# Performance work log

Hardware: AMD Instinct MI355X
Metric: run time of the kernel (lower is better)

The kernel has to match this reference:

```python
import jax, jax.numpy as jnp
import numpy as np

D_MODEL = 1024
D_HIDDEN = 4096
N_EXPERTS = 8
B, S = 2, 2048


def setup_inputs() -> dict:
    key = jax.random.key(0)
    ks = jax.random.split(key, 4)
    sd = 1.0 / np.sqrt(D_MODEL)
    sh = 1.0 / np.sqrt(D_HIDDEN)
    return {
        "x": jax.random.normal(ks[0], (B, S, D_MODEL), dtype=jnp.float32),
        "Wg": jax.random.normal(ks[1], (D_MODEL, N_EXPERTS), dtype=jnp.float32) * sd,
        "bg": jnp.zeros((N_EXPERTS,), dtype=jnp.float32),
        "W1": jax.random.normal(ks[2], (N_EXPERTS, D_MODEL, D_HIDDEN), dtype=jnp.float32) * sd,
        "b1": jnp.zeros((N_EXPERTS, D_HIDDEN), dtype=jnp.float32),
        "W2": jax.random.normal(ks[3], (N_EXPERTS, D_HIDDEN, D_MODEL), dtype=jnp.float32) * sh,
        "b2": jnp.zeros((N_EXPERTS, D_MODEL), dtype=jnp.float32),
    }


def reference(x, Wg, bg, W1, b1, W2, b2):
    # Router: softmax is monotone, so argmax(softmax(logits)) == argmax(logits).
    logits = jnp.einsum("bsd,de->bse", x, Wg) + bg
    expert_idx = jnp.argmax(logits, axis=-1)  # [B, S]
    # Top-1 dispatch, expressed as compute-all-experts + per-token select
    # (jit-friendly; the torch loop masks/gathers per expert).
    h = jax.nn.gelu(jnp.einsum("bsd,edh->bseh", x, W1) + b1, approximate=False)
    y = jnp.einsum("bseh,ehd->bsed", h, W2) + b2  # [B, S, E, D]
    out = jnp.take_along_axis(y, expert_idx[:, :, None, None], axis=2)[:, :, 0, :]
    return out
```

## Files before the change

### kernel.cpp

```cpp
#include <hip/hip_runtime.h>
#include <hip/hip_bf16.h>
#include <math.h>

#define D_MODEL 1024
#define D_HIDDEN 4096
#define N_EXP 8
#define N_TOK 4096
#define MBS 40

typedef __attribute__((ext_vector_type(8))) __bf16 bf16x8_t;
typedef __attribute__((ext_vector_type(4))) float f32x4_t;

#define WS_PREFIX_OFF 128
#define WS_BUCKET_OFF 256
#define WS_XB_OFF     ((size_t)1 << 18)
#define WS_HT_OFF     (((size_t)1 << 18) + ((size_t)8 << 20))
#define WS_W1T_OFF    (((size_t)1 << 18) + ((size_t)50 << 20))
#define WS_W2T_OFF    (((size_t)1 << 18) + ((size_t)114 << 20))
#define WS_AE_OFF     (((size_t)1 << 18) + ((size_t)178 << 20))
#define WS_NEED       (((size_t)1 << 18) + ((size_t)189 << 20))

__device__ __forceinline__ void gload16(const void* g, void* l) {
    __builtin_amdgcn_global_load_lds(
        (__attribute__((address_space(1))) void*)(g),
        (__attribute__((address_space(3))) void*)(l),
        16, 0, 0);
}

__global__ __launch_bounds__(64) void init_counts(int* counts) {
    if (threadIdx.x < N_EXP) counts[threadIdx.x] = 0;
}

__global__ __launch_bounds__(64) void prefix_kernel(const int* counts, int* prefix) {
    if (threadIdx.x == 0) {
        int s = 0;
        prefix[0] = 0;
#pragma unroll
        for (int e = 0; e < N_EXP; ++e) { s += (counts[e] + 127) >> 7; prefix[e + 1] = s; }
    }
}

__global__ __launch_bounds__(256) void router_kernel(
    const float* __restrict__ x, const float* __restrict__ Wg,
    const float* __restrict__ bg, int* __restrict__ counts,
    int* __restrict__ bucket, __hip_bfloat16* __restrict__ xb)
{
    const int wid  = threadIdx.x >> 6;
    const int lane = threadIdx.x & 63;
    const int t    = blockIdx.x * 4 + wid;
    const float* xr = x + (size_t)t * D_MODEL;

    double acc[N_EXP];
#pragma unroll
    for (int e = 0; e < N_EXP; ++e) acc[e] = 0.0;

#pragma unroll
    for (int j = 0; j < D_MODEL / 64; ++j) {
        const int d = j * 64 + lane;
        const float xv = xr[d];
        xb[(size_t)t * D_MODEL + d] = __float2bfloat16(xv);
        const float4* wr = (const float4*)(Wg + (size_t)d * N_EXP);
        const float4 w0 = wr[0], w1 = wr[1];
        const double xd = (double)xv;
        acc[0] += xd * (double)w0.x; acc[1] += xd * (double)w0.y;
        acc[2] += xd * (double)w0.z; acc[3] += xd * (double)w0.w;
        acc[4] += xd * (double)w1.x; acc[5] += xd * (double)w1.y;
        acc[6] += xd * (double)w1.z; acc[7] += xd * (double)w1.w;
    }
#pragma unroll
    for (int e = 0; e < N_EXP; ++e) {
        double v = acc[e];
#pragma unroll
        for (int off = 32; off >= 1; off >>= 1) v += __shfl_xor(v, off, 64);
        acc[e] = v + (double)bg[e];
    }
    if (lane == 0) {
        int best = 0; double bv = acc[0];
#pragma unroll
        for (int e = 1; e < N_EXP; ++e)
            if (acc[e] > bv) { bv = acc[e]; best = e; }
        const int pos = atomicAdd(&counts[best], 1);
        bucket[best * N_TOK + pos] = t;
    }
}

template<int KT, int NT>
__global__ __launch_bounds__(256) void convert_w(
    const float* __restrict__ W, __hip_bfloat16* __restrict__ Wt)
{
    constexpr int NB = NT / 128, KC = KT / 64;
    const int nblk = blockIdx.x, kc = blockIdx.y, e = blockIdx.z;
    const int k0 = kc * 64, n0 = nblk * 128;
    const int tid = threadIdx.x;
    __shared__ __hip_bfloat16 Lt[128 * 72];

    const int kr = tid >> 2;
    const int cq = tid & 3;
    const float* src = W + (size_t)e * KT * NT + (size_t)(k0 + kr) * NT + n0 + cq * 32;
#pragma unroll
    for (int f = 0; f < 8; ++f) {
        const float4 v = *(const float4*)(src + f * 4);
#pragma unroll
        for (int j = 0; j < 4; ++j) {
            const int n = cq * 32 + f * 4 + j;
            *(__hip_bfloat16*)((char*)Lt + (size_t)n * 144 + kr * 2) = __float2bfloat16(((const float*)&v)[j]);
        }
    }
    __syncthreads();

    char* outc = (char*)Wt + (((size_t)e * NB + nblk) * KC + kc) * 16384;
    const int n = tid >> 1, half = tid & 1;
#pragma unroll
    for (int s = 0; s < 4; ++s) {
        const int slot = half * 4 + s;
        const int ko = slot ^ (n & 7);
        const uint4 v = *(const uint4*)((const char*)Lt + (size_t)n * 144 + ko * 16);
        *(uint4*)(outc + (size_t)n * 128 + slot * 16) = v;
    }
}

__global__ __launch_bounds__(256) void gather_a(
    const float* __restrict__ x, const int* __restrict__ counts,
    const int* __restrict__ prefix, const int* __restrict__ bucket,
    __hip_bfloat16* __restrict__ Ae)
{
    const int mbg = blockIdx.x, kc = blockIdx.y;
    if (mbg >= prefix[8]) return;
    int e = 0;
#pragma unroll
    for (int q = 1; q < 8; ++q) if (mbg >= prefix[q]) e = q;
    const int cnt  = counts[e];
    const int mblk = mbg - prefix[e];
    const int tid  = threadIdx.x;
    const int m = tid >> 1, half = tid & 1;
    int idx = mblk * 128 + m;
    if (idx >= cnt) idx = cnt - 1;
    const int tok = bucket[e * N_TOK + idx];
    const float* src = x + (size_t)tok * D_MODEL + kc * 64 + half * 32;
    char* dst = (char*)Ae + ((size_t)mbg * 16 + kc) * 16384 + (size_t)m * 128;
#pragma unroll
    for (int s = 0; s < 4; ++s) {
        const float4 a = *(const float4*)(src + s * 8);
        const float4 b = *(const float4*)(src + s * 8 + 4);
        union { __hip_bfloat16 hh[8]; uint4 u; } pk;
#pragma unroll
        for (int j = 0; j < 4; ++j) {
            pk.hh[j]     = __float2bfloat16(((const float*)&a)[j]);
            pk.hh[j + 4] = __float2bfloat16(((const float*)&b)[j]);
        }
        const int ko = half * 4 + s;
        *(uint4*)(dst + ((ko ^ (m & 7)) << 4)) = pk.u;
    }
}

template<int K_TOT, int N_TOT, bool IS_FFN1>
__global__ __launch_bounds__(256, 4) void ffn_gemm_c(
    const __hip_bfloat16* __restrict__ At,
    const __hip_bfloat16* __restrict__ Wt,
    const float* __restrict__ bias,
    const int* __restrict__ counts,
    const int* __restrict__ prefix,
    const int* __restrict__ bucket,
    __hip_bfloat16* __restrict__ hout,
    float* __restrict__ yout)
{
    constexpr int NB  = N_TOT / 128;
    constexpr int KC  = K_TOT / 64;
    constexpr int NWG = MBS * NB;

    const int orig = blockIdx.x;
    const int wg   = (orig & 7) * (NWG >> 3) + (orig >> 3);
    const int nblk = wg / MBS;
    const int mbg  = wg % MBS;
    if (mbg >= prefix[8]) return;
    int e = 0;
#pragma unroll
    for (int q = 1; q < 8; ++q) if (mbg >= prefix[q]) e = q;
    const int cnt = counts[e];
    const int m0  = (mbg - prefix[e]) * 128;
    const int n0  = nblk * 128;

    const int tid  = threadIdx.x;
    const int lane = tid & 63;
    const int wid  = tid >> 6;
    const int wm   = wid >> 1, wn = wid & 1;

    __shared__ char As[16384];
    __shared__ char Bs[16384];
    __shared__ int s_tok[128];

    if (!IS_FFN1 && tid < 128) {
        int idx = m0 + tid;
        if (idx >= cnt) idx = cnt - 1;
        s_tok[tid] = bucket[e * N_TOK + idx];
    }

    const char* Abase = (const char*)At + (size_t)mbg * KC * 16384;
    const char* Bbase = (const char*)Wt + ((size_t)e * NB + nblk) * (size_t)KC * 16384;
    const int off  = wid * 4096 + lane * 16;
    char* lA = As + wid * 4096;
    char* lB = Bs + wid * 4096;

    f32x4_t acc[4][4];
#pragma unroll
    for (int f = 0; f < 4; ++f)
#pragma unroll
        for (int g = 0; g < 4; ++g) acc[f][g] = (f32x4_t){0.f, 0.f, 0.f, 0.f};

    for (int t = 0; t < KC; ++t) {
        const char* Ac = Abase + (size_t)t * 16384 + off;
        const char* Bc = Bbase + (size_t)t * 16384 + off;
#pragma unroll
        for (int i = 0; i < 4; ++i) gload16(Ac + i * 1024, lA + i * 1024);
#pragma unroll
        for (int i = 0; i < 4; ++i) gload16(Bc + i * 1024, lB + i * 1024);
        __syncthreads();

#pragma unroll
        for (int kk = 0; kk < 2; ++kk) {
            uint4 af[4], bf[4];
            const int ko = kk * 4 + (lane >> 4);
#pragma unroll
            for (int f = 0; f < 4; ++f) {
                const int r = wm * 64 + f * 16 + (lane & 15);
                af[f] = *(const uint4*)(As + r * 128 + ((ko ^ (r & 7)) << 4));
            }
#pragma unroll
            for (int g = 0; g < 4; ++g) {
                const int n = wn * 64 + g * 16 + (lane & 15);
                bf[g] = *(const uint4*)(Bs + n * 128 + ((ko ^ (n & 7)) << 4));
            }
#pragma unroll
            for (int f = 0; f < 4; ++f)
#pragma unroll
                for (int g = 0; g < 4; ++g)
                    acc[f][g] = __builtin_amdgcn_mfma_f32_16x16x32_bf16(
                        __builtin_bit_cast(bf16x8_t, af[f]),
                        __builtin_bit_cast(bf16x8_t, bf[g]),
                        acc[f][g], 0, 0, 0);
        }
        __syncthreads();
    }

    if (IS_FFN1) {
        char* hb = (char*)hout + (size_t)mbg * (D_HIDDEN / 64) * 16384;
#pragma unroll
        for (int f = 0; f < 4; ++f) {
#pragma unroll
            for (int j = 0; j < 4; ++j) {
                const int m = wm * 64 + f * 16 + (lane >> 4) * 4 + j;
#pragma unroll
                for (int g = 0; g < 4; ++g) {
                    const int col = n0 + wn * 64 + g * 16 + (lane & 15);
                    float v = acc[f][g][j] + bias[e * N_TOT + col];
                    v = 0.5f * v * (1.0f + erff(v * 0.70710678118654752f));
                    const int kc = col >> 6, kw = col & 63, ko = kw >> 3, b = kw & 7;
                    *(__hip_bfloat16*)(hb + ((size_t)kc * 128 + m) * 128 +
                                       (((ko ^ (m & 7)) << 4) + (b << 1))) = __float2bfloat16(v);
                }
            }
        }
    } else {
#pragma unroll
        for (int f = 0; f < 4; ++f) {
#pragma unroll
            for (int j = 0; j < 4; ++j) {
                const int rl = wm * 64 + f * 16 + (lane >> 4) * 4 + j;
                const bool ok = (m0 + rl) < cnt;
                const int tok = s_tok[rl];
#pragma unroll
                for (int g = 0; g < 4; ++g) {
                    const int col = n0 + wn * 64 + g * 16 + (lane & 15);
                    const float v = acc[f][g][j] + bias[e * N_TOT + col];
                    if (ok) yout[(size_t)tok * N_TOT + col] = v;
                }
            }
        }
    }
}

template<int K_TOT, int N_TOT, bool IS_FFN1>
__global__ __launch_bounds__(256, 2) void ffn_gemm_f32(
    const __hip_bfloat16* __restrict__ A,
    const float* __restrict__ W,
    const float* __restrict__ bias,
    const int* __restrict__ counts,
    const int* __restrict__ bucket,
    __hip_bfloat16* __restrict__ hout,
    float* __restrict__ yout)
{
    const int e   = blockIdx.z;
    const int cnt = counts[e];
    const int m0  = blockIdx.y * 128;
    if (m0 >= cnt) return;
    const int n0   = blockIdx.x * 128;
    const int tid  = threadIdx.x;
    const int lane = tid & 63;
    const int wid  = tid >> 6;
    const int wm   = wid >> 1, wn = wid & 1;

    __shared__ __hip_bfloat16 As[128 * 64];
    __shared__ __hip_bfloat16 Bs[128 * 64];
    __shared__ int s_tok[128];

    if (tid < 128) {
        int idx = m0 + tid;
        if (idx >= cnt) idx = cnt - 1;
        s_tok[tid] = bucket[e * N_TOK + idx];
    }
    __syncthreads();

    const __hip_bfloat16* gA[4]; char* lA[4];
#pragma unroll
    for (int i = 0; i < 4; ++i) {
        const int r = wid * 32 + i * 8 + (lane >> 3);
        gA[i] = A + (size_t)s_tok[r] * K_TOT + (((lane & 7) ^ (r & 7)) << 3);
        lA[i] = (char*)As + (size_t)(wid * 32 + i * 8) * 128;
    }
    const int ko_t = lane & 7;
    const int nq   = wid * 8 + (lane >> 3);
    const float* wb = W + (size_t)e * K_TOT * N_TOT + (size_t)(ko_t * 8) * N_TOT + n0 + nq * 4;

    f32x4_t acc[4][4];
#pragma unroll
    for (int f = 0; f < 4; ++f)
#pragma unroll
        for (int g = 0; g < 4; ++g) acc[f][g] = (f32x4_t){0.f, 0.f, 0.f, 0.f};

    for (int k0 = 0; k0 < K_TOT; k0 += 64) {
#pragma unroll
        for (int i = 0; i < 4; ++i) gload16(gA[i] + k0, lA[i]);
        const float* wk = wb + (size_t)k0 * N_TOT;
        float4 v[8];
#pragma unroll
        for (int j = 0; j < 8; ++j) v[j] = *(const float4*)(wk + (size_t)j * N_TOT);
#pragma unroll
        for (int i = 0; i < 4; ++i) {
            const int n = nq * 4 + i;
            union { __hip_bfloat16 hh[8]; uint4 u; } pk;
#pragma unroll
            for (int j = 0; j < 8; ++j) pk.hh[j] = __float2bfloat16(((const float*)&v[j])[i]);
            *(uint4*)((char*)Bs + n * 128 + ((ko_t ^ (n & 7)) << 4)) = pk.u;
        }
        __syncthreads();

#pragma unroll
        for (int kk = 0; kk < 2; ++kk) {
            uint4 af[4], bf[4];
            const int ko = kk * 4 + (lane >> 4);
#pragma unroll
            for (int f = 0; f < 4; ++f) {
                const int r = wm * 64 + f * 16 + (lane & 15);
                af[f] = *(const uint4*)((const char*)As + r * 128 + ((ko ^ (r & 7)) << 4));
            }
#pragma unroll
            for (int g = 0; g < 4; ++g) {
                const int n = wn * 64 + g * 16 + (lane & 15);
                bf[g] = *(const uint4*)((const char*)Bs + n * 128 + ((ko ^ (n & 7)) << 4));
            }
#pragma unroll
            for (int f = 0; f < 4; ++f)
#pragma unroll
                for (int g = 0; g < 4; ++g)
                    acc[f][g] = __builtin_amdgcn_mfma_f32_16x16x32_bf16(
                        __builtin_bit_cast(bf16x8_t, af[f]),
                        __builtin_bit_cast(bf16x8_t, bf[g]),
                        acc[f][g], 0, 0, 0);
        }
        __syncthreads();
    }

#pragma unroll
    for (int f = 0; f < 4; ++f) {
#pragma unroll
        for (int j = 0; j < 4; ++j) {
            const int rl = wm * 64 + f * 16 + (lane >> 4) * 4 + j;
            const bool ok = (m0 + rl) < cnt;
            const int tok = s_tok[rl];
#pragma unroll
            for (int g = 0; g < 4; ++g) {
                const int col = n0 + wn * 64 + g * 16 + (lane & 15);
                float v = acc[f][g][j] + bias[e * N_TOT + col];
                if (IS_FFN1) {
                    v = 0.5f * v * (1.0f + erff(v * 0.70710678118654752f));
                    if (ok) hout[(size_t)tok * N_TOT + col] = __float2bfloat16(v);
                } else {
                    if (ok) yout[(size_t)tok * N_TOT + col] = v;
                }
            }
        }
    }
}

extern "C" void kernel_launch(void* const* d_in, const int* in_sizes, int n_in,
                              void* d_out, int out_size, void* d_ws, size_t ws_size,
                              hipStream_t stream) {
    const float* x  = (const float*)d_in[0];
    const float* Wg = (const float*)d_in[1];
    const float* bg = (const float*)d_in[2];
    const float* W1 = (const float*)d_in[3];
    const float* b1 = (const float*)d_in[4];
    const float* W2 = (const float*)d_in[5];
    const float* b2 = (const float*)d_in[6];
    float* out = (float*)d_out;

    char* ws = (char*)d_ws;
    int* counts = (int*)(ws);
    int* prefix = (int*)(ws + WS_PREFIX_OFF);
    int* bucket = (int*)(ws + WS_BUCKET_OFF);
    __hip_bfloat16* xb  = (__hip_bfloat16*)(ws + WS_XB_OFF);
    __hip_bfloat16* ht  = (__hip_bfloat16*)(ws + WS_HT_OFF);
    __hip_bfloat16* w1t = (__hip_bfloat16*)(ws + WS_W1T_OFF);
    __hip_bfloat16* w2t = (__hip_bfloat16*)(ws + WS_W2T_OFF);
    __hip_bfloat16* ae  = (__hip_bfloat16*)(ws + WS_AE_OFF);

    init_counts<<<dim3(1), dim3(64), 0, stream>>>(counts);
    router_kernel<<<dim3(N_TOK / 4), dim3(256), 0, stream>>>(x, Wg, bg, counts, bucket, xb);
    prefix_kernel<<<dim3(1), dim3(64), 0, stream>>>(counts, prefix);

    if (ws_size >= WS_NEED) {
        convert_w<D_MODEL, D_HIDDEN><<<dim3(32, 16, N_EXP), dim3(256), 0, stream>>>(W1, w1t);
        convert_w<D_HIDDEN, D_MODEL><<<dim3(8, 64, N_EXP), dim3(256), 0, stream>>>(W2, w2t);
        gather_a<<<dim3(MBS, 16), dim3(256), 0, stream>>>(x, counts, prefix, bucket, ae);
        ffn_gemm_c<D_MODEL, D_HIDDEN, true>
            <<<dim3(MBS * (D_HIDDEN / 128)), dim3(256), 0, stream>>>(
                ae, w1t, b1, counts, prefix, bucket, ht, nullptr);
        ffn_gemm_c<D_HIDDEN, D_MODEL, false>
            <<<dim3(MBS * (D_MODEL / 128)), dim3(256), 0, stream>>>(
                ht, w2t, b2, counts, prefix, bucket, nullptr, out);
    } else {
        __hip_bfloat16* h = ht;
        ffn_gemm_f32<D_MODEL, D_HIDDEN, true>
            <<<dim3(D_HIDDEN / 128, N_TOK / 128, N_EXP), dim3(256), 0, stream>>>(
                xb, W1, b1, counts, bucket, h, nullptr);
        ffn_gemm_f32<D_HIDDEN, D_MODEL, false>
            <<<dim3(D_MODEL / 128, N_TOK / 128, N_EXP), dim3(256), 0, stream>>>(
                h, W2, b2, counts, bucket, nullptr, out);
    }
}
```

Before: 321.7 us.

## Widen GEMM tiles to 128x256, split-K FFN2 with reduce kernel, vectorize weight convert

The grouped expert GEMMs now use 128x256 output tiles, so each A tile loaded into LDS is reused across twice as many columns, and occupancy is lowered to 2 blocks per CU. FFN2 is split across K into two partial-sum buffers, reusing the W1 scratch region, and a new reduce kernel adds the partials plus bias and scatters rows to token positions. The weight conversion kernel now reads four rows at once and writes packed 8-byte LDS stores with a tighter row pitch. The trade-off is extra partial-buffer traffic, an additional launch, and higher register pressure from the 4x8 accumulator array.

After: 333.8 us. 3.8% more time.

```diff
diff --git a/kernel.cpp b/kernel.cpp
--- a/kernel.cpp
+++ b/kernel.cpp
@@ -92,18 +92,27 @@
     const int nblk = blockIdx.x, kc = blockIdx.y, e = blockIdx.z;
     const int k0 = kc * 64, n0 = nblk * 128;
     const int tid = threadIdx.x;
-    __shared__ __hip_bfloat16 Lt[128 * 72];
-
-    const int kr = tid >> 2;
-    const int cq = tid & 3;
-    const float* src = W + (size_t)e * KT * NT + (size_t)(k0 + kr) * NT + n0 + cq * 32;
-#pragma unroll
-    for (int f = 0; f < 8; ++f) {
-        const float4 v = *(const float4*)(src + f * 4);
-#pragma unroll
-        for (int j = 0; j < 4; ++j) {
-            const int n = cq * 32 + f * 4 + j;
-            *(__hip_bfloat16*)((char*)Lt + (size_t)n * 144 + kr * 2) = __float2bfloat16(((const float*)&v)[j]);
+    __shared__ __hip_bfloat16 Lt[128 * 68];
+
+    const int nq  = tid & 31;
+    const int kq2 = tid >> 5;
+#pragma unroll
+    for (int h = 0; h < 2; ++h) {
+        const int kq = kq2 + h * 8;
+        const float* src = W + (size_t)e * KT * NT + (size_t)(k0 + kq * 4) * NT + n0 + nq * 4;
+        const float4 v0 = *(const float4*)(src);
+        const float4 v1 = *(const float4*)(src + (size_t)NT);
+        const float4 v2 = *(const float4*)(src + (size_t)2 * NT);
+        const float4 v3 = *(const float4*)(src + (size_t)3 * NT);
+#pragma unroll
+        for (int i = 0; i < 4; ++i) {
+            const int n = nq * 4 + i;
+            union { __hip_bfloat16 hh[4]; unsigned long long u; } pk;
+            pk.hh[0] = __float2bfloat16(((const float*)&v0)[i]);
+            pk.hh[1] = __float2bfloat16(((const float*)&v1)[i]);
+            pk.hh[2] = __float2bfloat16(((const float*)&v2)[i]);
+            pk.hh[3] = __float2bfloat16(((const float*)&v3)[i]);
+            *(unsigned long long*)((char*)Lt + (size_t)n * 136 + kq * 8) = pk.u;
         }
     }
     __syncthreads();
@@ -114,7 +123,7 @@
     for (int s = 0; s < 4; ++s) {
         const int slot = half * 4 + s;
         const int ko = slot ^ (n & 7);
-        const uint4 v = *(const uint4*)((const char*)Lt + (size_t)n * 144 + ko * 16);
+        const uint4 v = *(const uint4*)((const char*)Lt + (size_t)n * 136 + ko * 16);
         *(uint4*)(outc + (size_t)n * 128 + slot * 16) = v;
     }
 }
@@ -153,32 +162,33 @@
     }
 }
 
-template<int K_TOT, int N_TOT, bool IS_FFN1>
-__global__ __launch_bounds__(256, 4) void ffn_gemm_c(
+template<int K_TOT, int N_TOT, int SPLITS, bool IS_FFN1>
+__global__ __launch_bounds__(256, 2) void ffn_gemm_w(
     const __hip_bfloat16* __restrict__ At,
     const __hip_bfloat16* __restrict__ Wt,
     const float* __restrict__ bias,
     const int* __restrict__ counts,
     const int* __restrict__ prefix,
-    const int* __restrict__ bucket,
     __hip_bfloat16* __restrict__ hout,
-    float* __restrict__ yout)
-{
-    constexpr int NB  = N_TOT / 128;
-    constexpr int KC  = K_TOT / 64;
-    constexpr int NWG = MBS * NB;
+    float* __restrict__ pout)
+{
+    constexpr int KC     = K_TOT / 64;
+    constexpr int KSTEPS = KC / SPLITS;
+    constexpr int NBW    = N_TOT / 256;
+    constexpr int NB128  = N_TOT / 128;
+    constexpr int NWG    = NBW * SPLITS * MBS;
 
     const int orig = blockIdx.x;
     const int wg   = (orig & 7) * (NWG >> 3) + (orig >> 3);
-    const int nblk = wg / MBS;
-    const int mbg  = wg % MBS;
+    const int nblk = wg / (SPLITS * MBS);
+    const int r2   = wg % (SPLITS * MBS);
+    const int split = r2 / MBS;
+    const int mbg   = r2 % MBS;
     if (mbg >= prefix[8]) return;
     int e = 0;
 #pragma unroll
     for (int q = 1; q < 8; ++q) if (mbg >= prefix[q]) e = q;
-    const int cnt = counts[e];
-    const int m0  = (mbg - prefix[e]) * 128;
-    const int n0  = nblk * 128;
+    const int n0 = nblk * 256;
 
     const int tid  = threadIdx.x;
     const int lane = tid & 63;
@@ -186,39 +196,37 @@
     const int wm   = wid >> 1, wn = wid & 1;
 
     __shared__ char As[16384];
-    __shared__ char Bs[16384];
-    __shared__ int s_tok[128];
-
-    if (!IS_FFN1 && tid < 128) {
-        int idx = m0 + tid;
-        if (idx >= cnt) idx = cnt - 1;
-        s_tok[tid] = bucket[e * N_TOK + idx];
-    }
-
-    const char* Abase = (const char*)At + (size_t)mbg * KC * 16384;
-    const char* Bbase = (const char*)Wt + ((size_t)e * NB + nblk) * (size_t)KC * 16384;
-    const int off  = wid * 4096 + lane * 16;
-    char* lA = As + wid * 4096;
-    char* lB = Bs + wid * 4096;
-
-    f32x4_t acc[4][4];
+    __shared__ char Bs[32768];
+
+    const char* Ab  = (const char*)At + ((size_t)mbg * KC + split * KSTEPS) * 16384;
+    const char* Bb0 = (const char*)Wt + (((size_t)e * NB128 + nblk * 2) * KC + split * KSTEPS) * 16384;
+    const char* Bb1 = Bb0 + (size_t)KC * 16384;
+    const int off = wid * 4096 + lane * 16;
+    char* lA  = As + wid * 4096;
+    char* lB0 = Bs + wid * 4096;
+    char* lB1 = Bs + 16384 + wid * 4096;
+
+    f32x4_t acc[4][8];
 #pragma unroll
     for (int f = 0; f < 4; ++f)
 #pragma unroll
-        for (int g = 0; g < 4; ++g) acc[f][g] = (f32x4_t){0.f, 0.f, 0.f, 0.f};
-
-    for (int t = 0; t < KC; ++t) {
-        const char* Ac = Abase + (size_t)t * 16384 + off;
-        const char* Bc = Bbase + (size_t)t * 16384 + off;
+        for (int g = 0; g < 8; ++g) acc[f][g] = (f32x4_t){0.f, 0.f, 0.f, 0.f};
+
+    for (int t = 0; t < KSTEPS; ++t) {
+        const char* Ac = Ab  + (size_t)t * 16384 + off;
+        const char* B0 = Bb0 + (size_t)t * 16384 + off;
+        const char* B1 = Bb1 + (size_t)t * 16384 + off;
 #pragma unroll
         for (int i = 0; i < 4; ++i) gload16(Ac + i * 1024, lA + i * 1024);
 #pragma unroll
-        for (int i = 0; i < 4; ++i) gload16(Bc + i * 1024, lB + i * 1024);
+        for (int i = 0; i < 4; ++i) gload16(B0 + i * 1024, lB0 + i * 1024);
+#pragma unroll
+        for (int i = 0; i < 4; ++i) gload16(B1 + i * 1024, lB1 + i * 1024);
         __syncthreads();
 
 #pragma unroll
         for (int kk = 0; kk < 2; ++kk) {
-            uint4 af[4], bf[4];
+            uint4 af[4], bf[8];
             const int ko = kk * 4 + (lane >> 4);
 #pragma unroll
             for (int f = 0; f < 4; ++f) {
@@ -226,14 +234,14 @@
                 af[f] = *(const uint4*)(As + r * 128 + ((ko ^ (r & 7)) << 4));
             }
 #pragma unroll
-            for (int g = 0; g < 4; ++g) {
-                const int n = wn * 64 + g * 16 + (lane & 15);
+            for (int g = 0; g < 8; ++g) {
+                const int n = wn * 128 + g * 16 + (lane & 15);
                 bf[g] = *(const uint4*)(Bs + n * 128 + ((ko ^ (n & 7)) << 4));
             }
 #pragma unroll
             for (int f = 0; f < 4; ++f)
 #pragma unroll
-                for (int g = 0; g < 4; ++g)
+                for (int g = 0; g < 8; ++g)
                     acc[f][g] = __builtin_amdgcn_mfma_f32_16x16x32_bf16(
                         __builtin_bit_cast(bf16x8_t, af[f]),
                         __builtin_bit_cast(bf16x8_t, bf[g]),
@@ -250,8 +258,8 @@
             for (int j = 0; j < 4; ++j) {
                 const int m = wm * 64 + f * 16 + (lane >> 4) * 4 + j;
 #pragma unroll
-                for (int g = 0; g < 4; ++g) {
-                    const int col = n0 + wn * 64 + g * 16 + (lane & 15);
+                for (int g = 0; g < 8; ++g) {
+                    const int col = n0 + wn * 128 + g * 16 + (lane & 15);
                     float v = acc[f][g][j] + bias[e * N_TOT + col];
                     v = 0.5f * v * (1.0f + erff(v * 0.70710678118654752f));
                     const int kc = col >> 6, kw = col & 63, ko = kw >> 3, b = kw & 7;
@@ -261,21 +269,53 @@
             }
         }
     } else {
+        float* pb = pout + ((size_t)(split * MBS + mbg) * 128) * 1024;
 #pragma unroll
         for (int f = 0; f < 4; ++f) {
 #pragma unroll
             for (int j = 0; j < 4; ++j) {
-                const int rl = wm * 64 + f * 16 + (lane >> 4) * 4 + j;
-                const bool ok = (m0 + rl) < cnt;
-                const int tok = s_tok[rl];
-#pragma unroll
-                for (int g = 0; g < 4; ++g) {
-                    const int col = n0 + wn * 64 + g * 16 + (lane & 15);
-                    const float v = acc[f][g][j] + bias[e * N_TOT + col];
-                    if (ok) yout[(size_t)tok * N_TOT + col] = v;
+                const int m = wm * 64 + f * 16 + (lane >> 4) * 4 + j;
+#pragma unroll
+                for (int g = 0; g < 8; ++g) {
+                    const int col = n0 + wn * 128 + g * 16 + (lane & 15);
+                    pb[(size_t)m * 1024 + col] = acc[f][g][j];
                 }
             }
         }
+    }
+}
+
+__global__ __launch_bounds__(256) void reduce_out(
+    const float* __restrict__ P, const float* __restrict__ b2,
+    const int* __restrict__ counts, const int* __restrict__ prefix,
+    const int* __restrict__ bucket, float* __restrict__ out)
+{
+    const int slot = blockIdx.x;
+    if (slot >= prefix[8]) return;
+    int e = 0;
+#pragma unroll
+    for (int q = 1; q < 8; ++q) if (slot >= prefix[q]) e = q;
+    const int cnt  = counts[e];
+    const int mblk = slot - prefix[e];
+    const int r    = blockIdx.y * 4 + (threadIdx.x >> 6);
+    const int idx  = mblk * 128 + r;
+    if (idx >= cnt) return;
+    const int tok  = bucket[e * N_TOK + idx];
+    const int lane = threadIdx.x & 63;
+    const float* p0 = P + ((size_t)slot * 128 + r) * 1024;
+    const float* p1 = P + ((size_t)(MBS + slot) * 128 + r) * 1024;
+    const float* bb = b2 + e * 1024;
+    float* op = out + (size_t)tok * 1024;
+#pragma unroll
+    for (int j = 0; j < 4; ++j) {
+        const int c = j * 256 + lane * 4;
+        const float4 a = *(const float4*)(p0 + c);
+        const float4 b = *(const float4*)(p1 + c);
+        const float4 w = *(const float4*)(bb + c);
+        float4 v;
+        v.x = a.x + b.x + w.x; v.y = a.y + b.y + w.y;
+        v.z = a.z + b.z + w.z; v.w = a.w + b.w + w.w;
+        *(float4*)(op + c) = v;
     }
 }
 
@@ -413,6 +453,7 @@
     __hip_bfloat16* w1t = (__hip_bfloat16*)(ws + WS_W1T_OFF);
     __hip_bfloat16* w2t = (__hip_bfloat16*)(ws + WS_W2T_OFF);
     __hip_bfloat16* ae  = (__hip_bfloat16*)(ws + WS_AE_OFF);
+    float* partials     = (float*)(ws + WS_W1T_OFF);
 
     init_counts<<<dim3(1), dim3(64), 0, stream>>>(counts);
     router_kernel<<<dim3(N_TOK / 4), dim3(256), 0, stream>>>(x, Wg, bg, counts, bucket, xb);
@@ -422,12 +463,14 @@
         convert_w<D_MODEL, D_HIDDEN><<<dim3(32, 16, N_EXP), dim3(256), 0, stream>>>(W1, w1t);
         convert_w<D_HIDDEN, D_MODEL><<<dim3(8, 64, N_EXP), dim3(256), 0, stream>>>(W2, w2t);
         gather_a<<<dim3(MBS, 16), dim3(256), 0, stream>>>(x, counts, prefix, bucket, ae);
-        ffn_gemm_c<D_MODEL, D_HIDDEN, true>
-            <<<dim3(MBS * (D_HIDDEN / 128)), dim3(256), 0, stream>>>(
-                ae, w1t, b1, counts, prefix, bucket, ht, nullptr);
-        ffn_gemm_c<D_HIDDEN, D_MODEL, false>
-            <<<dim3(MBS * (D_MODEL / 128)), dim3(256), 0, stream>>>(
-                ht, w2t, b2, counts, prefix, bucket, nullptr, out);
+        ffn_gemm_w<D_MODEL, D_HIDDEN, 1, true>
+            <<<dim3(MBS * (D_HIDDEN / 256)), dim3(256), 0, stream>>>(
+                ae, w1t, b1, counts, prefix, ht, nullptr);
+        ffn_gemm_w<D_HIDDEN, D_MODEL, 2, false>
+            <<<dim3(MBS * (D_MODEL / 256) * 2), dim3(256), 0, stream>>>(
+                ht, w2t, nullptr, counts, prefix, nullptr, partials);
+        reduce_out<<<dim3(MBS, 32), dim3(256), 0, stream>>>(
+            partials, b2, counts, prefix, bucket, out);
     } else {
         __hip_bfloat16* h = ht;
         ffn_gemm_f32<D_MODEL, D_HIDDEN, true>
```
